# Kernel optimization log

Hardware: AMD Instinct MI355X
Metric: run time of the kernel (lower is better)

Reference implementation:

```python
import jax, jax.numpy as jnp
import numpy as np

B, V, M, L, D, OUT = 16, 16, 32, 24, 128, 193
VOCAB = {'cond': 5000, 'proc': 2000, 'drug': 600, 'lab_item': 700, 'lab_value': 200, 'inj_item': 400, 'inj_value': 200}


def setup_inputs() -> dict:
    key = jax.random.key(0)
    ks = iter(jax.random.split(key, 48))
    def emb_table(v):
        t = 0.02 * jax.random.normal(next(ks), (v, D), jnp.float32)
        return t.at[0].set(0.0)  # padding_idx = 0
    inp = {}
    inp['tok_cond'] = jax.random.randint(next(ks), (B, V, L), 0, VOCAB['cond'])
    inp['tok_proc'] = jax.random.randint(next(ks), (B, V, L), 0, VOCAB['proc'])
    inp['tok_drug'] = jax.random.randint(next(ks), (B, V, L), 0, VOCAB['drug'])
    inp['tok_lab_item'] = jax.random.randint(next(ks), (B, V, M, L), 0, VOCAB['lab_item'])
    inp['tok_lab_value'] = jax.random.randint(next(ks), (B, V, M, L), 0, VOCAB['lab_value'])
    inp['tok_inj_item'] = jax.random.randint(next(ks), (B, V, M, L), 0, VOCAB['inj_item'])
    inp['tok_inj_value'] = jax.random.randint(next(ks), (B, V, M, L), 0, VOCAB['inj_value'])
    inp['weight'] = jax.random.uniform(next(ks), (B, V, 1), jnp.float32)
    inp['age'] = jax.random.uniform(next(ks), (B, V, 1), jnp.float32)
    for n in ['cond', 'proc', 'drug', 'lab_item', 'lab_value', 'inj_item', 'inj_value']:
        inp['emb_' + n] = emb_table(VOCAB[n])
    def gru_params(nk):
        s = 0.05
        return (s * jax.random.normal(next(ks), (nk, 3 * D, D), jnp.float32),
                s * jax.random.normal(next(ks), (nk, 3 * D, D), jnp.float32),
                jnp.zeros((nk, 3 * D), jnp.float32),
                jnp.zeros((nk, 3 * D), jnp.float32))
    inp['mgru_wih'], inp['mgru_whh'], inp['mgru_bih'], inp['mgru_bhh'] = gru_params(5)
    inp['vgru_wih'], inp['vgru_whh'], inp['vgru_bih'], inp['vgru_bhh'] = gru_params(7)
    inp['info_w'] = 0.05 * jax.random.normal(next(ks), (2, D), jnp.float32)  # Linear(1, D) weights for weight/age
    inp['info_b'] = jnp.zeros((2, D), jnp.float32)
    inp['fc_w'] = 0.05 * jax.random.normal(next(ks), (7 * D, OUT), jnp.float32)
    inp['fc_b'] = jnp.zeros((OUT,), jnp.float32)
    return inp


def _gru(x, wih, whh, bih, bhh):
    # x: [N, T, Din]; torch nn.GRU semantics, gate order (r, z, n), h0 = 0
    n_, t_, _ = x.shape
    d = whh.shape[1]
    xg = jnp.einsum('ntd,gd->ntg', x, wih) + bih  # precompute input gates [N, T, 3D]
    def step(h, xg_t):
        gh = h @ whh.T + bhh
        ir, iz, inn = jnp.split(xg_t, 3, axis=-1)
        hr, hz, hn = jnp.split(gh, 3, axis=-1)
        r = jax.nn.sigmoid(ir + hr)
        z = jax.nn.sigmoid(iz + hz)
        n = jnp.tanh(inn + r * hn)
        h2 = (1.0 - z) * n + z * h
        return h2, h2
    h0 = jnp.zeros((n_, d), x.dtype)
    hT, outs = jax.lax.scan(step, h0, jnp.swapaxes(xg, 0, 1))
    return jnp.swapaxes(outs, 0, 1), hT  # output [N,T,D], hidden [N,D]

_gru_keys = jax.vmap(_gru)  # vmap over the per-feature-key leading axis


def reference(tok_cond, tok_proc, tok_drug, tok_lab_item, tok_lab_value, tok_inj_item, tok_inj_value,
              weight, age, emb_cond, emb_proc, emb_drug, emb_lab_item, emb_lab_value, emb_inj_item,
              emb_inj_value, mgru_wih, mgru_whh, mgru_bih, mgru_bhh, vgru_wih, vgru_whh, vgru_bih,
              vgru_bhh, info_w, info_b, fc_w, fc_b):
    b, v, m, _ = tok_lab_item.shape
    d = emb_cond.shape[1]
    # visit-event features: embedding + sum over code dim (dropout = identity, eval mode)
    e_cond = emb_cond[tok_cond].sum(axis=2)  # [B,V,D]
    e_proc = emb_proc[tok_proc].sum(axis=2)
    e_drug = emb_drug[tok_drug].sum(axis=2)
    # monitor-event pairs: elementwise mul of the two embeddings, sum over code dim
    lab = (emb_lab_item[tok_lab_item] * emb_lab_value[tok_lab_value]).sum(axis=3)  # [B,V,M,D]
    inj = (emb_inj_item[tok_inj_item] * emb_inj_value[tok_inj_value]).sum(axis=3)
    # repeat visit embeddings across the monitor axis (repeat(1, max_monitors, 1))
    rep = lambda e: jnp.broadcast_to(e[:, :, None, :], (b, v, m, d))
    mon_in = jnp.stack([rep(e_cond), rep(e_proc), rep(e_drug), lab, inj], axis=0)
    mon_in = mon_in.reshape(5, b * v, m, d)  # aggregate_tensors with uniform lengths
    # per-key monitor-level GRUs
    mon_out, mon_h = _gru_keys(mon_in, mgru_wih, mgru_whh, mgru_bih, mgru_bhh)
    # split_tensor + extract_and_transpose: take last monitor step per visit -> [5,B,V,D]
    last = mon_out[:, :, -1, :].reshape(5, b, v, d)
    # patient info Linear(1, D) for weight / age
    w_emb = weight * info_w[0] + info_b[0]  # [B,V,D]
    a_emb = age * info_w[1] + info_b[1]
    vis_in = jnp.concatenate([last, jnp.stack([w_emb, a_emb], axis=0)], axis=0)  # [7,B,V,D]
    # per-key visit-level GRUs
    _, vis_h = _gru_keys(vis_in, vgru_wih, vgru_whh, vgru_bih, vgru_bhh)  # [7,B,D]
    patient_emb = jnp.transpose(vis_h, (1, 0, 2)).reshape(b, 7 * d)  # concatenate_patient_embeddings
    logits = jax.nn.relu(patient_emb) @ fc_w + fc_b  # fc_patient: ReLU -> Linear(7D, output_size)
    return logits
```

## Files before the change

### kernel.cpp

```cpp
#include <hip/hip_runtime.h>
#include <stdint.h>

typedef unsigned short u16;
typedef unsigned int u32;

#define B_ 16
#define V_ 16
#define M_ 32
#define L_ 24
#define D_ 128
#define G_ 384
#define N_ 256
#define NM_ 8192
#define OUT_ 193

using bf16x8 = __attribute__((ext_vector_type(8))) __bf16;
using floatx4 = __attribute__((ext_vector_type(4))) float;
using u16x4 = __attribute__((ext_vector_type(4))) u16;

__device__ __forceinline__ float bf2f(u16 u) {
  u32 x = ((u32)u) << 16;
  return __builtin_bit_cast(float, x);
}
__device__ __forceinline__ u16 f2bf(float f) {
  u32 u = __builtin_bit_cast(u32, f);
  u = (u + 0x7FFFu + ((u >> 16) & 1u)) >> 16;
  return (u16)u;
}
__device__ __forceinline__ float sigm_(float x) {
  return __builtin_amdgcn_rcpf(1.0f + __expf(-x));
}
__device__ __forceinline__ float tanh_(float x) {
  float e = __expf(2.0f * x);
  return 1.0f - 2.0f * __builtin_amdgcn_rcpf(e + 1.0f);
}
__device__ __forceinline__ floatx4 mfma16(bf16x8 a, bf16x8 b, floatx4 c) {
  return __builtin_amdgcn_mfma_f32_16x16x32_bf16(a, b, c, 0, 0, 0);
}
__device__ __forceinline__ void lds_barrier() {
  asm volatile("s_waitcnt lgkmcnt(0)\n\ts_barrier" ::: "memory");
}

__device__ __forceinline__ void split4(floatx4 v, u16* __restrict__ hip, u16* __restrict__ lop) {
  u16x4 h, l;
#pragma unroll
  for (int k = 0; k < 4; k++) {
    u16 hb = f2bf(v[k]);
    h[k] = hb;
    l[k] = f2bf(v[k] - bf2f(hb));
  }
  *(u16x4*)hip = h;
  *(u16x4*)lop = l;
}

#define CONVB 1152
#define VEB 32
#define PEB 1024

__global__ __launch_bounds__(256) void k_stage1(
    const int* __restrict__ tc, const int* __restrict__ tp, const int* __restrict__ td,
    const int* __restrict__ tli, const int* __restrict__ tlv,
    const int* __restrict__ tii, const int* __restrict__ tiv,
    const float* __restrict__ ec, const float* __restrict__ ep, const float* __restrict__ ed,
    const float* __restrict__ eli, const float* __restrict__ elv,
    const float* __restrict__ eii, const float* __restrict__ eiv,
    const float* __restrict__ wv, const float* __restrict__ av,
    const float* __restrict__ iw, const float* __restrict__ ib,
    const float* __restrict__ mwih, const float* __restrict__ vwih,
    const float* __restrict__ mwhh, const float* __restrict__ vwhh,
    u16* __restrict__ wih_hi, u16* __restrict__ whh_hi,
    u16* __restrict__ ce_hi, u16* __restrict__ ce_lo,
    u16* __restrict__ vx_hi, u16* __restrict__ vx_lo,
    u16* __restrict__ mx_hi, u16* __restrict__ mx_lo) {
  int blk = blockIdx.x, tid = threadIdx.x;
  if (blk < CONVB) {
    const int SW = 12 * G_ * D_, S5 = 5 * G_ * D_;
    int i4 = (blk * 256 + tid) * 4;
    floatx4 v;
    u16* dst;
    if (i4 < SW) {
      v = *(const floatx4*)(i4 < S5 ? mwih + i4 : vwih + (i4 - S5));
      dst = wih_hi + i4;
    } else {
      int o = i4 - SW;
      v = *(const floatx4*)(o < S5 ? mwhh + o : vwhh + (o - S5));
      dst = whh_hi + o;
    }
    u16x4 h;
#pragma unroll
    for (int k = 0; k < 4; k++) h[k] = f2bf(v[k]);
    *(u16x4*)dst = h;
  } else if (blk < CONVB + VEB) {
    int n = (blk - CONVB) * 8 + (tid >> 5);
    int j = tid & 31;
    floatx4 a0 = {0.f, 0.f, 0.f, 0.f}, a1 = a0, a2 = a0;
#pragma unroll 4
    for (int l = 0; l < L_; l++) {
      a0 += *(const floatx4*)(ec + (size_t)tc[n * L_ + l] * D_ + j * 4);
      a1 += *(const floatx4*)(ep + (size_t)tp[n * L_ + l] * D_ + j * 4);
      a2 += *(const floatx4*)(ed + (size_t)td[n * L_ + l] * D_ + j * 4);
    }
    size_t o0 = (size_t)n * D_ + j * 4;
    split4(a0, ce_hi + o0, ce_lo + o0);
    split4(a1, ce_hi + (size_t)N_ * D_ + o0, ce_lo + (size_t)N_ * D_ + o0);
    split4(a2, ce_hi + (size_t)2 * N_ * D_ + o0, ce_lo + (size_t)2 * N_ * D_ + o0);
    float wq = wv[n], aq = av[n];
    floatx4 iw0 = *(const floatx4*)(iw + j * 4);
    floatx4 iw1 = *(const floatx4*)(iw + D_ + j * 4);
    floatx4 ib0 = *(const floatx4*)(ib + j * 4);
    floatx4 ib1 = *(const floatx4*)(ib + D_ + j * 4);
    floatx4 v1 = wq * iw0 + ib0;
    floatx4 v2 = aq * iw1 + ib1;
    split4(v1, vx_hi + (size_t)5 * N_ * D_ + o0, vx_lo + (size_t)5 * N_ * D_ + o0);
    split4(v2, vx_hi + (size_t)6 * N_ * D_ + o0, vx_lo + (size_t)6 * N_ * D_ + o0);
  } else {
    int r = (blk - CONVB - VEB) * 8 + (tid >> 5);
    int j = tid & 31;
    floatx4 al4 = {0.f, 0.f, 0.f, 0.f}, ai4 = al4;
#pragma unroll 4
    for (int l = 0; l < L_; l++) {
      al4 += *(const floatx4*)(eli + (size_t)tli[r * L_ + l] * D_ + j * 4) *
             *(const floatx4*)(elv + (size_t)tlv[r * L_ + l] * D_ + j * 4);
      ai4 += *(const floatx4*)(eii + (size_t)tii[r * L_ + l] * D_ + j * 4) *
             *(const floatx4*)(eiv + (size_t)tiv[r * L_ + l] * D_ + j * 4);
    }
    size_t o = (size_t)r * D_ + j * 4;
    split4(al4, mx_hi + o, mx_lo + o);
    split4(ai4, mx_hi + (size_t)NM_ * D_ + o, mx_lo + (size_t)NM_ * D_ + o);
  }
}

template <int MODE, int TT>
__global__ __launch_bounds__(512, 1) void k_gru8(
    int cpk,
    const u16* __restrict__ xa_hi, const u16* __restrict__ xa_lo,
    const u16* __restrict__ xb_hi, const u16* __restrict__ xb_lo,
    const u16* __restrict__ wih_all, const float* __restrict__ bih_all,
    const u16* __restrict__ whh_all, const float* __restrict__ bhh_all,
    u16* __restrict__ out_hi, u16* __restrict__ out_lo, float* __restrict__ out_f32) {
  int key = blockIdx.x / cpk;
  int chunk = blockIdx.x - key * cpk;
  int n0 = chunk * 16;
  const u16* whh = whh_all + (size_t)key * (G_ * D_);
  const u16* wih = wih_all + (size_t)key * (G_ * D_);

  __shared__ __align__(16) u16 hls[2][2][16 * 128];

  int tid = threadIdx.x;
  int w = tid >> 6, lane = tid & 63, mq = lane & 15, q = lane >> 4;
  int dA = (w << 4) + mq;

  const bool constx = (MODE == 0) && (key < 3);
  const u16 *xhb, *xlb;
  size_t xbase, TS;
  if (MODE == 0) {
    if (key < 3) { xhb = xa_hi; xlb = xa_lo; xbase = ((size_t)key * N_ + n0 + mq) * D_; TS = 0; }
    else { xhb = xb_hi; xlb = xb_lo; xbase = ((size_t)(key - 3) * NM_ + (size_t)(n0 + mq) * M_) * D_; TS = D_; }
  } else {
    xhb = xa_hi; xlb = xa_lo; xbase = ((size_t)key * N_ + mq * 16) * D_; TS = D_;
  }

  bf16x8 bw[3][4], wf[3][4];
#pragma unroll
  for (int g = 0; g < 3; g++)
#pragma unroll
    for (int kk = 0; kk < 4; kk++) {
      size_t ro = (size_t)(g * 128 + dA) * D_ + kk * 32 + q * 8;
      bw[g][kk] = *(const bf16x8*)(whh + ro);
      wf[g][kk] = *(const bf16x8*)(wih + ro);
    }
  floatx4 bseed[3], bxs[3];
#pragma unroll
  for (int g = 0; g < 3; g++) {
    float bh = bhh_all[key * G_ + g * 128 + dA];
    float bi = bih_all[key * G_ + g * 128 + dA];
    bseed[g] = {bh, bh, bh, bh};
    bxs[g] = {bi, bi, bi, bi};
  }

  bf16x8 xh[4], xl[4];
#pragma unroll
  for (int kk = 0; kk < 4; kk++) {
    xh[kk] = *(const bf16x8*)(xhb + xbase + kk * 32 + q * 8);
    xl[kk] = *(const bf16x8*)(xlb + xbase + kk * 32 + q * 8);
  }

  floatx4 accx[3];
  if (constx) {
#pragma unroll
    for (int g = 0; g < 3; g++) {
      floatx4 a = mfma16(xh[0], wf[g][0], bxs[g]);
      a = mfma16(xl[0], wf[g][0], a);
      a = mfma16(xh[1], wf[g][1], a);
      a = mfma16(xl[1], wf[g][1], a);
      a = mfma16(xh[2], wf[g][2], a);
      a = mfma16(xl[2], wf[g][2], a);
      a = mfma16(xh[3], wf[g][3], a);
      accx[g] = mfma16(xl[3], wf[g][3], a);
    }
  }

  float h_old[4];
#pragma unroll
  for (int k = 0; k < 4; k++) h_old[k] = 0.f;

#pragma unroll 2
  for (int t = 0; t < TT; ++t) {
    if (!constx) {
#pragma unroll
      for (int g = 0; g < 3; g++) {
        floatx4 a = mfma16(xh[0], wf[g][0], bxs[g]);
        a = mfma16(xl[0], wf[g][0], a);
        a = mfma16(xh[1], wf[g][1], a);
        a = mfma16(xl[1], wf[g][1], a);
        a = mfma16(xh[2], wf[g][2], a);
        a = mfma16(xl[2], wf[g][2], a);
        a = mfma16(xh[3], wf[g][3], a);
        accx[g] = mfma16(xl[3], wf[g][3], a);
      }
      if (t + 1 < TT) {
        size_t xo = xbase + (size_t)(t + 1) * TS;
#pragma unroll
        for (int kk = 0; kk < 4; kk++) {
          xh[kk] = *(const bf16x8*)(xhb + xo + kk * 32 + q * 8);
          xl[kk] = *(const bf16x8*)(xlb + xo + kk * 32 + q * 8);
        }
      }
    }
    floatx4 acch[3];
    if (t > 0) {
      const u16* hp0 = &hls[(t - 1) & 1][0][0];
      const u16* hp1 = &hls[(t - 1) & 1][1][0];
      bf16x8 ah[4], al[4];
#pragma unroll
      for (int kk = 0; kk < 4; kk++) {
        int off = mq * 128 + (((kk * 4 + q) ^ mq) * 8);
        ah[kk] = *(const bf16x8*)(hp0 + off);
        al[kk] = *(const bf16x8*)(hp1 + off);
      }
#pragma unroll
      for (int g = 0; g < 3; g++) {
        floatx4 a = mfma16(ah[0], bw[g][0], bseed[g]);
        a = mfma16(al[0], bw[g][0], a);
        a = mfma16(ah[1], bw[g][1], a);
        a = mfma16(al[1], bw[g][1], a);
        a = mfma16(ah[2], bw[g][2], a);
        a = mfma16(al[2], bw[g][2], a);
        a = mfma16(ah[3], bw[g][3], a);
        acch[g] = mfma16(al[3], bw[g][3], a);
      }
    } else {
#pragma unroll
      for (int g = 0; g < 3; g++) acch[g] = bseed[g];
    }
    u16* wrh = &hls[t & 1][0][0];
    u16* wrl = &hls[t & 1][1][0];
#pragma unroll
    for (int i = 0; i < 4; i++) {
      int row = q * 4 + i;
      float r = sigm_(accx[0][i] + acch[0][i]);
      float z = sigm_(accx[1][i] + acch[1][i]);
      float nn = tanh_(accx[2][i] + r * acch[2][i]);
      float h2 = (1.0f - z) * nn + z * h_old[i];
      h_old[i] = h2;
      u32 ub = __builtin_bit_cast(u32, h2);
      u16 hb = (u16)(ub >> 16);
      float rem = h2 - __builtin_bit_cast(float, ub & 0xFFFF0000u);
      u16 lb = f2bf(rem);
      if (t == TT - 1) {
        if (MODE == 0) {
          size_t o = ((size_t)key * N_ + n0 + row) * D_ + dA;
          out_hi[o] = hb;
          out_lo[o] = lb;
        } else {
          out_f32[((size_t)key * 16 + row) * D_ + dA] = h2;
        }
      } else {
        int idx = row * 128 + (((dA >> 3) ^ row) * 8) + (dA & 7);
        wrh[idx] = hb;
        wrl[idx] = lb;
      }
    }
    if (t + 1 < TT) lds_barrier();
  }
}

__global__ __launch_bounds__(256) void k_fc(
    const float* __restrict__ vis_h, const float* __restrict__ fc_w,
    const float* __restrict__ fc_b, float* __restrict__ out) {
  int b = blockIdx.x;
  int cg = blockIdx.y;
  int tid = threadIdx.x;
  int j = tid & 15, s = tid >> 4;
  int c = cg * 16 + j;
  bool cv = c < OUT_;

  __shared__ float hbuf[7 * D_];
  __shared__ float red[16][16];
  for (int i = tid; i < 7 * D_; i += 256) {
    float v = vis_h[((size_t)(i >> 7) * 16 + b) * D_ + (i & 127)];
    hbuf[i] = v > 0.f ? v : 0.f;
  }
  __syncthreads();

  float acc = 0.f;
  if (cv) {
    const float* wp = fc_w + (size_t)(s * 56) * OUT_ + c;
#pragma unroll 8
    for (int k = 0; k < 56; k++) acc += hbuf[s * 56 + k] * wp[(size_t)k * OUT_];
  }
  red[s][j] = acc;
  __syncthreads();
  if (s == 0 && cv) {
    float t = 0.f;
#pragma unroll
    for (int m = 0; m < 16; m++) t += red[m][j];
    out[(size_t)b * OUT_ + c] = t + fc_b[c];
  }
}

extern "C" void kernel_launch(void* const* d_in, const int* in_sizes, int n_in,
                              void* d_out, int out_size, void* d_ws, size_t ws_size,
                              hipStream_t stream) {
  (void)in_sizes; (void)n_in; (void)out_size; (void)ws_size;
  const int* tok_cond = (const int*)d_in[0];
  const int* tok_proc = (const int*)d_in[1];
  const int* tok_drug = (const int*)d_in[2];
  const int* tok_lab_item = (const int*)d_in[3];
  const int* tok_lab_value = (const int*)d_in[4];
  const int* tok_inj_item = (const int*)d_in[5];
  const int* tok_inj_value = (const int*)d_in[6];
  const float* weight = (const float*)d_in[7];
  const float* age = (const float*)d_in[8];
  const float* emb_cond = (const float*)d_in[9];
  const float* emb_proc = (const float*)d_in[10];
  const float* emb_drug = (const float*)d_in[11];
  const float* emb_lab_item = (const float*)d_in[12];
  const float* emb_lab_value = (const float*)d_in[13];
  const float* emb_inj_item = (const float*)d_in[14];
  const float* emb_inj_value = (const float*)d_in[15];
  const float* mgru_wih = (const float*)d_in[16];
  const float* mgru_whh = (const float*)d_in[17];
  const float* mgru_bih = (const float*)d_in[18];
  const float* mgru_bhh = (const float*)d_in[19];
  const float* vgru_wih = (const float*)d_in[20];
  const float* vgru_whh = (const float*)d_in[21];
  const float* vgru_bih = (const float*)d_in[22];
  const float* vgru_bhh = (const float*)d_in[23];
  const float* info_w = (const float*)d_in[24];
  const float* info_b = (const float*)d_in[25];
  const float* fc_w = (const float*)d_in[26];
  const float* fc_b = (const float*)d_in[27];

  char* p = (char*)d_ws;
  auto take = [&](size_t bytes) { char* r = p; p += (bytes + 255) & ~(size_t)255; return r; };
  u16* mx_hi = (u16*)take((size_t)2 * NM_ * D_ * 2);
  u16* mx_lo = (u16*)take((size_t)2 * NM_ * D_ * 2);
  u16* ce_hi = (u16*)take((size_t)3 * N_ * D_ * 2);
  u16* ce_lo = (u16*)take((size_t)3 * N_ * D_ * 2);
  u16* vx_hi = (u16*)take((size_t)7 * N_ * D_ * 2);
  u16* vx_lo = (u16*)take((size_t)7 * N_ * D_ * 2);
  float* vis_h = (float*)take((size_t)7 * 16 * D_ * 4);
  u16* wih_hi = (u16*)take((size_t)12 * G_ * D_ * 2);
  u16* whh_hi = (u16*)take((size_t)12 * G_ * D_ * 2);

  k_stage1<<<CONVB + VEB + PEB, 256, 0, stream>>>(
      tok_cond, tok_proc, tok_drug, tok_lab_item, tok_lab_value, tok_inj_item, tok_inj_value,
      emb_cond, emb_proc, emb_drug, emb_lab_item, emb_lab_value, emb_inj_item, emb_inj_value,
      weight, age, info_w, info_b, mgru_wih, vgru_wih, mgru_whh, vgru_whh,
      wih_hi, whh_hi, ce_hi, ce_lo, vx_hi, vx_lo, mx_hi, mx_lo);
  k_gru8<0, 32><<<80, 512, 0, stream>>>(16, ce_hi, ce_lo, mx_hi, mx_lo,
                                        wih_hi, mgru_bih, whh_hi, mgru_bhh,
                                        vx_hi, vx_lo, nullptr);
  k_gru8<1, 16><<<7, 512, 0, stream>>>(1, vx_hi, vx_lo, nullptr, nullptr,
                                       wih_hi + (size_t)5 * G_ * D_, vgru_bih,
                                       whh_hi + (size_t)5 * G_ * D_, vgru_bhh,
                                       nullptr, nullptr, vis_h);
  k_fc<<<dim3(B_, 13), 256, 0, stream>>>(vis_h, fc_w, fc_b, (float*)d_out);
}
```

Before: 265.8 us.

## Split GRU MFMA chains into hi/lo accumulators and double-buffer input prefetch two steps ahead

Each 8-long dependent MFMA chain per gate becomes two independent 4-long chains (hi and lo parts), summed at the end, to shorten the serial MFMA latency on the recurrent critical path. The time loop is manually unrolled by two with A/B input register buffers, so x for step t+2 is prefetched instead of t+1. The LDS h loads are issued before the input-projection MFMAs to hide LDS latency. This costs extra registers for the second input buffer and the extra accumulators, and the loop assumes TT is even (M=32 and V=16 both are).

After: 409.7 us. +54.2%, slower.

```diff
diff --git a/kernel.cpp b/kernel.cpp
--- a/kernel.cpp
+++ b/kernel.cpp
@@ -177,26 +177,35 @@
     bseed[g] = {bh, bh, bh, bh};
     bxs[g] = {bi, bi, bi, bi};
   }
-
-  bf16x8 xh[4], xl[4];
+  const floatx4 fzero = {0.f, 0.f, 0.f, 0.f};
+
+  bf16x8 xhA[4], xlA[4], xhB[4], xlB[4];
 #pragma unroll
   for (int kk = 0; kk < 4; kk++) {
-    xh[kk] = *(const bf16x8*)(xhb + xbase + kk * 32 + q * 8);
-    xl[kk] = *(const bf16x8*)(xlb + xbase + kk * 32 + q * 8);
+    xhA[kk] = *(const bf16x8*)(xhb + xbase + kk * 32 + q * 8);
+    xlA[kk] = *(const bf16x8*)(xlb + xbase + kk * 32 + q * 8);
+  }
+  if (!constx) {
+#pragma unroll
+    for (int kk = 0; kk < 4; kk++) {
+      xhB[kk] = *(const bf16x8*)(xhb + xbase + TS + kk * 32 + q * 8);
+      xlB[kk] = *(const bf16x8*)(xlb + xbase + TS + kk * 32 + q * 8);
+    }
   }
 
   floatx4 accx[3];
   if (constx) {
 #pragma unroll
     for (int g = 0; g < 3; g++) {
-      floatx4 a = mfma16(xh[0], wf[g][0], bxs[g]);
-      a = mfma16(xl[0], wf[g][0], a);
-      a = mfma16(xh[1], wf[g][1], a);
-      a = mfma16(xl[1], wf[g][1], a);
-      a = mfma16(xh[2], wf[g][2], a);
-      a = mfma16(xl[2], wf[g][2], a);
-      a = mfma16(xh[3], wf[g][3], a);
-      accx[g] = mfma16(xl[3], wf[g][3], a);
+      floatx4 axh = mfma16(xhA[0], wf[g][0], bxs[g]);
+      axh = mfma16(xhA[1], wf[g][1], axh);
+      axh = mfma16(xhA[2], wf[g][2], axh);
+      axh = mfma16(xhA[3], wf[g][3], axh);
+      floatx4 axl = mfma16(xlA[0], wf[g][0], fzero);
+      axl = mfma16(xlA[1], wf[g][1], axl);
+      axl = mfma16(xlA[2], wf[g][2], axl);
+      axl = mfma16(xlA[3], wf[g][3], axl);
+      accx[g] = axh + axl;
     }
   }
 
@@ -204,85 +213,91 @@
 #pragma unroll
   for (int k = 0; k < 4; k++) h_old[k] = 0.f;
 
-#pragma unroll 2
-  for (int t = 0; t < TT; ++t) {
-    if (!constx) {
-#pragma unroll
-      for (int g = 0; g < 3; g++) {
-        floatx4 a = mfma16(xh[0], wf[g][0], bxs[g]);
-        a = mfma16(xl[0], wf[g][0], a);
-        a = mfma16(xh[1], wf[g][1], a);
-        a = mfma16(xl[1], wf[g][1], a);
-        a = mfma16(xh[2], wf[g][2], a);
-        a = mfma16(xl[2], wf[g][2], a);
-        a = mfma16(xh[3], wf[g][3], a);
-        accx[g] = mfma16(xl[3], wf[g][3], a);
-      }
-      if (t + 1 < TT) {
-        size_t xo = xbase + (size_t)(t + 1) * TS;
-#pragma unroll
-        for (int kk = 0; kk < 4; kk++) {
-          xh[kk] = *(const bf16x8*)(xhb + xo + kk * 32 + q * 8);
-          xl[kk] = *(const bf16x8*)(xlb + xo + kk * 32 + q * 8);
-        }
-      }
-    }
-    floatx4 acch[3];
-    if (t > 0) {
-      const u16* hp0 = &hls[(t - 1) & 1][0][0];
-      const u16* hp1 = &hls[(t - 1) & 1][1][0];
-      bf16x8 ah[4], al[4];
-#pragma unroll
-      for (int kk = 0; kk < 4; kk++) {
-        int off = mq * 128 + (((kk * 4 + q) ^ mq) * 8);
-        ah[kk] = *(const bf16x8*)(hp0 + off);
-        al[kk] = *(const bf16x8*)(hp1 + off);
-      }
-#pragma unroll
-      for (int g = 0; g < 3; g++) {
-        floatx4 a = mfma16(ah[0], bw[g][0], bseed[g]);
-        a = mfma16(al[0], bw[g][0], a);
-        a = mfma16(ah[1], bw[g][1], a);
-        a = mfma16(al[1], bw[g][1], a);
-        a = mfma16(ah[2], bw[g][2], a);
-        a = mfma16(al[2], bw[g][2], a);
-        a = mfma16(ah[3], bw[g][3], a);
-        acch[g] = mfma16(al[3], bw[g][3], a);
-      }
-    } else {
-#pragma unroll
-      for (int g = 0; g < 3; g++) acch[g] = bseed[g];
-    }
-    u16* wrh = &hls[t & 1][0][0];
-    u16* wrl = &hls[t & 1][1][0];
-#pragma unroll
-    for (int i = 0; i < 4; i++) {
-      int row = q * 4 + i;
-      float r = sigm_(accx[0][i] + acch[0][i]);
-      float z = sigm_(accx[1][i] + acch[1][i]);
-      float nn = tanh_(accx[2][i] + r * acch[2][i]);
-      float h2 = (1.0f - z) * nn + z * h_old[i];
-      h_old[i] = h2;
-      u32 ub = __builtin_bit_cast(u32, h2);
-      u16 hb = (u16)(ub >> 16);
-      float rem = h2 - __builtin_bit_cast(float, ub & 0xFFFF0000u);
-      u16 lb = f2bf(rem);
-      if (t == TT - 1) {
-        if (MODE == 0) {
-          size_t o = ((size_t)key * N_ + n0 + row) * D_ + dA;
-          out_hi[o] = hb;
-          out_lo[o] = lb;
-        } else {
-          out_f32[((size_t)key * 16 + row) * D_ + dA] = h2;
-        }
-      } else {
-        int idx = row * 128 + (((dA >> 3) ^ row) * 8) + (dA & 7);
-        wrh[idx] = hb;
-        wrl[idx] = lb;
-      }
-    }
-    if (t + 1 < TT) lds_barrier();
-  }
+#define GRU_STEP(T, XH, XL)                                                                \
+  {                                                                                        \
+    const int t = (T);                                                                     \
+    bf16x8 ah[4], al[4];                                                                   \
+    if (t > 0) {                  \
+      const u16* hp0 = &hls[(t - 1) & 1][0][0];                                            \
+      const u16* hp1 = &hls[(t - 1) & 1][1][0];                                            \
+      _Pragma("unroll") for (int kk = 0; kk < 4; kk++) {                                   \
+        int off = mq * 128 + (((kk * 4 + q) ^ mq) * 8);                                    \
+        ah[kk] = *(const bf16x8*)(hp0 + off);                                              \
+        al[kk] = *(const bf16x8*)(hp1 + off);                                              \
+      }                                                                                    \
+    }                                                                                      \
+    if (!constx) {                                                                         \
+      _Pragma("unroll") for (int g = 0; g < 3; g++) {                                      \
+        floatx4 axh = mfma16(XH[0], wf[g][0], bxs[g]);                                     \
+        axh = mfma16(XH[1], wf[g][1], axh);                                                \
+        axh = mfma16(XH[2], wf[g][2], axh);                                                \
+        axh = mfma16(XH[3], wf[g][3], axh);                                                \
+        floatx4 axl = mfma16(XL[0], wf[g][0], fzero);                                      \
+        axl = mfma16(XL[1], wf[g][1], axl);                                                \
+        axl = mfma16(XL[2], wf[g][2], axl);                                                \
+        axl = mfma16(XL[3], wf[g][3], axl);                                                \
+        accx[g] = axh + axl;                                                               \
+      }                                                                                    \
+      if (t + 2 < TT) {                 \
+        size_t xo = xbase + (size_t)(t + 2) * TS;                                          \
+        _Pragma("unroll") for (int kk = 0; kk < 4; kk++) {                                 \
+          XH[kk] = *(const bf16x8*)(xhb + xo + kk * 32 + q * 8);                           \
+          XL[kk] = *(const bf16x8*)(xlb + xo + kk * 32 + q * 8);                           \
+        }                                                                                  \
+      }                                                                                    \
+    }                                                                                      \
+    floatx4 acch[3];                                                                       \
+    if (t > 0) {                                                                           \
+      _Pragma("unroll") for (int g = 0; g < 3; g++) {                                      \
+        floatx4 hhi = mfma16(ah[0], bw[g][0], bseed[g]);                                   \
+        hhi = mfma16(ah[1], bw[g][1], hhi);                                                \
+        hhi = mfma16(ah[2], bw[g][2], hhi);                                                \
+        hhi = mfma16(ah[3], bw[g][3], hhi);                                                \
+        floatx4 hlo = mfma16(al[0], bw[g][0], fzero);                                      \
+        hlo = mfma16(al[1], bw[g][1], hlo);                                                \
+        hlo = mfma16(al[2], bw[g][2], hlo);                                                \
+        hlo = mfma16(al[3], bw[g][3], hlo);                                                \
+        acch[g] = hhi + hlo;                                                               \
+      }                                                                                    \
+    } else {                                                                               \
+      _Pragma("unroll") for (int g = 0; g < 3; g++) acch[g] = bseed[g];                    \
+    }                                                                                      \
+    u16* wrh = &hls[t & 1][0][0];                                                          \
+    u16* wrl = &hls[t & 1][1][0];                                                          \
+    _Pragma("unroll") for (int i = 0; i < 4; i++) {                                        \
+      int row = q * 4 + i;                                                                 \
+      float r = sigm_(accx[0][i] + acch[0][i]);                                            \
+      float z = sigm_(accx[1][i] + acch[1][i]);                                            \
+      float nn = tanh_(accx[2][i] + r * acch[2][i]);                                       \
+      float h2 = (1.0f - z) * nn + z * h_old[i];                                           \
+      h_old[i] = h2;                                                                       \
+      u32 ub = __builtin_bit_cast(u32, h2);                                                \
+      u16 hb = (u16)(ub >> 16);                                                            \
+      float rem = h2 - __builtin_bit_cast(float, ub & 0xFFFF0000u);                        \
+      u16 lb = f2bf(rem);                                                                  \
+      if (t == TT - 1) {                                                                   \
+        if (MODE == 0) {                                                                   \
+          size_t o = ((size_t)key * N_ + n0 + row) * D_ + dA;                              \
+          out_hi[o] = hb;                                                                  \
+          out_lo[o] = lb;                                                                  \
+        } else {                                                                           \
+          out_f32[((size_t)key * 16 + row) * D_ + dA] = h2;                                \
+        }                                                                                  \
+      } else {                                                                             \
+        int idx = row * 128 + (((dA >> 3) ^ row) * 8) + (dA & 7);                          \
+        wrh[idx] = hb;                                                                     \
+        wrl[idx] = lb;                                                                     \
+      }                                                                                    \
+    }                                                                                      \
+    if (t + 1 < TT) lds_barrier();                                                         \
+  }
+
+#pragma unroll 1
+  for (int tb = 0; tb < TT; tb += 2) {
+    GRU_STEP(tb, xhA, xlA)
+    GRU_STEP(tb + 1, xhB, xlB)
+  }
+#undef GRU_STEP
 }
 
 __global__ __launch_bounds__(256) void k_fc(
```
